# Optimization experiments

Hardware: AMD Instinct MI355X
Metric: run time of the kernel (lower is better)

## Reference

```python
import jax, jax.numpy as jnp
import numpy as np

N = 50000      # nodes
E = 1600000    # edges (avg degree 32)
D = 64         # d_node
DE = 32        # d_edge
H = 4          # heads
L = 3          # layers


def _ln(x, g, b):
    mu = x.mean(-1, keepdims=True)
    var = ((x - mu) ** 2).mean(-1, keepdims=True)
    return (x - mu) / jnp.sqrt(var + 1e-5) * g + b


def setup_inputs() -> dict:
    key = jax.random.key(0)
    ks = jax.random.split(key, 16)
    s = 0.05
    return {
        "node_features": jax.random.normal(ks[0], (N, D), jnp.float32),
        "edge_features": jax.random.normal(ks[1], (E, DE), jnp.float32),
        "edge_index": jax.random.randint(ks[2], (2, E), 0, N),
        "Wq": jax.random.normal(ks[3], (L, D, D), jnp.float32) * s,
        "Wk": jax.random.normal(ks[4], (L, D, D), jnp.float32) * s,
        "Wv": jax.random.normal(ks[5], (L, D, D), jnp.float32) * s,
        "Wo": jax.random.normal(ks[6], (L, D, D), jnp.float32) * s,
        "We": jax.random.normal(ks[7], (L, DE, H), jnp.float32) * s,   # edge-conditioned score bias
        "Wem": jax.random.normal(ks[8], (L, 2 * D + DE, DE), jnp.float32) * s,
        "bem": jnp.zeros((L, DE), jnp.float32),
        "gn": jnp.ones((L, D), jnp.float32),
        "bn": jnp.zeros((L, D), jnp.float32),
        "ge": jnp.ones((L, DE), jnp.float32),
        "be": jnp.zeros((L, DE), jnp.float32),
    }


def _delta_forward(h, e, src, dst, Wq, Wk, Wv, Wo, We, Wem, bem, gn, bn, ge, be):
    n = h.shape[0]
    dh = D // H
    for i in range(L):
        # --- node attention over edges (sparse, per-dst segment softmax) ---
        q = (h @ Wq[i]).reshape(n, H, dh)
        k = (h @ Wk[i]).reshape(n, H, dh)
        v = (h @ Wv[i]).reshape(n, H, dh)
        scores = jnp.einsum('ehd,ehd->eh', q[dst], k[src]) / jnp.sqrt(jnp.float32(dh))
        scores = scores + e @ We[i]                         # edge-conditioned bias [E,H]
        m = jax.ops.segment_max(scores, dst, num_segments=n)
        p = jnp.exp(scores - m[dst])
        denom = jax.ops.segment_sum(p, dst, num_segments=n)
        alpha = p / (denom[dst] + 1e-9)                      # [E,H]
        msg = (alpha[:, :, None] * v[src]).reshape(-1, D)    # [E,D]
        agg = jax.ops.segment_sum(msg, dst, num_segments=n)  # [N,D]
        h = _ln(h + agg @ Wo[i], gn[i], bn[i])
        # --- edge update conditioned on endpoint nodes ---
        emsg = jax.nn.gelu(jnp.concatenate([h[src], h[dst], e], axis=-1) @ Wem[i] + bem[i])
        e = _ln(e + emsg, ge[i], be[i])
    return h


def reference(node_features, edge_features, edge_index, Wq, Wk, Wv, Wo, We, Wem, bem, gn, bn, ge, be):
    src = edge_index[0]
    dst = edge_index[1]
    return _delta_forward(node_features, edge_features, src, dst,
                          Wq, Wk, Wv, Wo, We, Wem, bem, gn, bn, ge, be)
```

## Files before the change

### kernel.cpp

```cpp
#include <hip/hip_runtime.h>
#include <hip/hip_bf16.h>
#include <math.h>

#define NN 50000
#define NE 1600000
#define D 64
#define DE 32
#define H 4
#define DH 16
#define L 3

typedef __attribute__((ext_vector_type(8))) short bf16x8;
typedef __attribute__((ext_vector_type(8))) short s16x8;
typedef __attribute__((ext_vector_type(4))) float f32x4;

__device__ __forceinline__ short f2b(float f) {
    __hip_bfloat16 h = __float2bfloat16(f);
    short s;
    __builtin_memcpy(&s, &h, 2);
    return s;
}
__device__ __forceinline__ float b2f(unsigned short u) {
    unsigned int x = ((unsigned int)u) << 16;
    float f; __builtin_memcpy(&f, &x, 4); return f;
}
__device__ __forceinline__ float b2f_lo(unsigned int p) {
    unsigned int x = p << 16;
    float f; __builtin_memcpy(&f, &x, 4); return f;
}
__device__ __forceinline__ float b2f_hi(unsigned int p) {
    unsigned int x = p & 0xffff0000u;
    float f; __builtin_memcpy(&f, &x, 4); return f;
}


__global__ void deg_kernel(const int* __restrict__ dst, int* __restrict__ cnt) {
    int e = blockIdx.x * 256 + threadIdx.x;
    if (e >= NE) return;
    atomicAdd(&cnt[dst[e]], 1);
}

__global__ void block_sum_kernel(const int* __restrict__ cnt, int* __restrict__ bsum) {
    int b = blockIdx.x, t = threadIdx.x;
    int base = b * 1024 + t * 4;
    int s = 0;
#pragma unroll
    for (int i = 0; i < 4; i++) { int idx = base + i; if (idx < NN) s += cnt[idx]; }
#pragma unroll
    for (int off = 32; off; off >>= 1) s += __shfl_down(s, off);
    __shared__ int wsum[4];
    if ((t & 63) == 0) wsum[t >> 6] = s;
    __syncthreads();
    if (t == 0) bsum[b] = wsum[0] + wsum[1] + wsum[2] + wsum[3];
}

__global__ void scan_bsum_kernel(int* __restrict__ bsum, int nb) {
    if (blockIdx.x == 0 && threadIdx.x == 0) {
        int run = 0;
        for (int i = 0; i < nb; i++) { int c = bsum[i]; bsum[i] = run; run += c; }
    }
}

__global__ void scan_block_kernel(const int* __restrict__ cnt, const int* __restrict__ bsum,
                                  int* __restrict__ offsets) {
    int b = blockIdx.x, t = threadIdx.x;
    int base = b * 1024 + t * 4;
    int v[4]; int s = 0;
#pragma unroll
    for (int i = 0; i < 4; i++) { int idx = base + i; v[i] = (idx < NN) ? cnt[idx] : 0; s += v[i]; }
    int lane = t & 63, w = t >> 6;
    int x = s;
#pragma unroll
    for (int off = 1; off < 64; off <<= 1) {
        int y = __shfl_up(x, off);
        if (lane >= off) x += y;
    }
    __shared__ int wsum[4];
    if (lane == 63) wsum[w] = x;
    __syncthreads();
    int woff = 0;
    for (int i = 0; i < w; i++) woff += wsum[i];
    int run = bsum[b] + woff + x - s;
#pragma unroll
    for (int i = 0; i < 4; i++) {
        int idx = base + i;
        if (idx < NN) offsets[idx] = run;
        run += v[i];
    }
}

__global__ void scatter_kernel(const int* __restrict__ src, const int* __restrict__ dst,
                               const int* __restrict__ offsets,
                               int* __restrict__ cursor,
                               int* __restrict__ sorted_eid,
                               int* __restrict__ sorted_src,
                               int* __restrict__ sorted_dst) {
    int e = blockIdx.x * 256 + threadIdx.x;
    if (e >= NE) return;
    int d0 = dst[e];
    int pos = atomicAdd(&cursor[d0], 1);
    int position = offsets[d0] + pos;
    sorted_eid[position] = e;
    sorted_src[position] = src[e];
    sorted_dst[position] = d0;
}

__global__ void eperm_kernel(const float* __restrict__ e32, const int* __restrict__ sorted_eid,
                             const float* __restrict__ We0,
                             unsigned short* __restrict__ eb_s,
                             float* __restrict__ ebias_s) {
    int t = blockIdx.x * 256 + threadIdx.x;
    if (t >= NE * 4) return;
    int p = t >> 2;
    int c = (t & 3) * 8;
    int eid = sorted_eid[p];
    const float* ep = e32 + (size_t)eid * DE + c;
    float4 x0 = *(const float4*)(ep);
    float4 x1 = *(const float4*)(ep + 4);
    float e8[8] = {x0.x, x0.y, x0.z, x0.w, x1.x, x1.y, x1.z, x1.w};
    s16x8 ob;
#pragma unroll
    for (int i = 0; i < 8; i++) ob[i] = f2b(e8[i]);
    *(s16x8*)(eb_s + (size_t)p * DE + c) = ob;
    float p0 = 0.f, p1 = 0.f, p2 = 0.f, p3 = 0.f;
#pragma unroll
    for (int i = 0; i < 8; i++) {
        float4 w = *(const float4*)(We0 + (c + i) * 4);
        p0 += e8[i] * w.x; p1 += e8[i] * w.y; p2 += e8[i] * w.z; p3 += e8[i] * w.w;
    }
#pragma unroll
    for (int off = 1; off < 4; off <<= 1) {
        p0 += __shfl_xor(p0, off, 4);
        p1 += __shfl_xor(p1, off, 4);
        p2 += __shfl_xor(p2, off, 4);
        p3 += __shfl_xor(p3, off, 4);
    }
    if ((t & 3) == 0) {
        float4 o; o.x = p0; o.y = p1; o.z = p2; o.w = p3;
        *(float4*)(ebias_s + (size_t)p * H) = o;
    }
}

__global__ void wconv_kernel(const float* __restrict__ Wem, unsigned short* __restrict__ Wt) {
    int t = blockIdx.x * 256 + threadIdx.x;
    if (t >= L * 32 * 160) return;
    int l = t / 5120;
    int r = t % 5120;
    int n = r / 160;
    int k = r % 160;
    Wt[t] = (unsigned short)f2b(Wem[l * 5120 + k * 32 + n]);
}

__global__ void hconv_kernel(const float* __restrict__ nf, float* __restrict__ h,
                             unsigned short* __restrict__ hb) {
    int t = blockIdx.x * 256 + threadIdx.x;
    if (t >= NN * D) return;
    float x = nf[t];
    h[t] = x;
    hb[t] = (unsigned short)f2b(x);
}


__global__ void qkv_kernel(const float* __restrict__ h,
                           const float* __restrict__ Wq,
                           const float* __restrict__ Wk,
                           const float* __restrict__ Wv,
                           float* __restrict__ q, unsigned int* __restrict__ kv) {
    __shared__ float sW[3 * 4096];
    __shared__ float sh[16][D];
    int col = threadIdx.x;
    int wv = threadIdx.y;
    int tid = wv * 64 + col;
    int base = blockIdx.x * 16;
    for (int i = tid; i < 4096; i += 256) {
        sW[i] = Wq[i]; sW[4096 + i] = Wk[i]; sW[8192 + i] = Wv[i];
    }
    for (int i = tid; i < 16 * D; i += 256) {
        int n = base + (i >> 6);
        sh[i >> 6][i & 63] = h[n * D + (i & 63)];
    }
    __syncthreads();
#pragma unroll
    for (int it = 0; it < 4; it++) {
        int ln = wv * 4 + it;
        int node = base + ln;
        float aq = 0.f, ak = 0.f, av = 0.f;
#pragma unroll
        for (int kk = 0; kk < D; kk++) {
            float hv = sh[ln][kk];
            aq += hv * sW[kk * D + col];
            ak += hv * sW[4096 + kk * D + col];
            av += hv * sW[8192 + kk * D + col];
        }
        q[node * D + col] = aq * 0.25f;
        unsigned int kb = (unsigned int)(unsigned short)f2b(ak);
        unsigned int vb = (unsigned int)(unsigned short)f2b(av);
        kv[node * D + col] = (vb << 16) | kb;
    }
}

__global__ void attn_kernel(const float* __restrict__ q, const unsigned int* __restrict__ kv,
                            const float* __restrict__ ebias_s,
                            const int* __restrict__ sorted_src,
                            const int* __restrict__ offsets,
                            float* __restrict__ agg) {
    int node = blockIdx.x * 4 + threadIdx.y;
    node = __builtin_amdgcn_readfirstlane(node);
    if (node >= NN) return;
    int lane = threadIdx.x;
    int hh = lane >> 4;
    float qv = q[node * D + lane];
    int beg = offsets[node];
    int end = (node == NN - 1) ? NE : offsets[node + 1];
    float mmax = -INFINITY, den = 0.f, acc = 0.f;
    int i = beg;
    for (; i + 8 <= end; i += 8) {
        int ss[8]; unsigned int kk8[8]; float bb8[8], dd[8];
#pragma unroll
        for (int u = 0; u < 8; u++) ss[u] = sorted_src[i + u];
#pragma unroll
        for (int u = 0; u < 8; u++) kk8[u] = kv[ss[u] * D + lane];
#pragma unroll
        for (int u = 0; u < 8; u++) bb8[u] = ebias_s[(i + u) * H + hh];
#pragma unroll
        for (int u = 0; u < 8; u++) dd[u] = qv * b2f_lo(kk8[u]);
#pragma unroll
        for (int off = 1; off < 16; off <<= 1) {
#pragma unroll
            for (int u = 0; u < 8; u++) dd[u] += __shfl_xor(dd[u], off, 16);
        }
        float nm = mmax;
#pragma unroll
        for (int u = 0; u < 8; u++) { dd[u] += bb8[u]; nm = fmaxf(nm, dd[u]); }
        float scale = __expf(mmax - nm);
        float ps = 0.f, av = 0.f;
#pragma unroll
        for (int u = 0; u < 8; u++) {
            float p = __expf(dd[u] - nm);
            ps += p;
            av += p * b2f_hi(kk8[u]);
        }
        den = den * scale + ps;
        acc = acc * scale + av;
        mmax = nm;
    }
    for (; i < end; i++) {
        int s = sorted_src[i];
        unsigned int kvv = kv[s * D + lane];
        float b = ebias_s[i * H + hh];
        float dot = qv * b2f_lo(kvv);
#pragma unroll
        for (int off = 1; off < 16; off <<= 1) dot += __shfl_xor(dot, off, 16);
        float score = dot + b;
        float nm = fmaxf(mmax, score);
        float scale = __expf(mmax - nm);
        float p = __expf(score - nm);
        den = den * scale + p;
        acc = acc * scale + p * b2f_hi(kvv);
        mmax = nm;
    }
    agg[node * D + lane] = acc / (den + 1e-9f);
}

__global__ void node_update_kernel(float* __restrict__ h, const float* __restrict__ agg,
                                   const float* __restrict__ Wo,
                                   const float* __restrict__ gn,
                                   const float* __restrict__ bn,
                                   unsigned short* __restrict__ hb) {
    __shared__ float sWo[4096];
    __shared__ float sagg[16][D];
    int col = threadIdx.x, wv = threadIdx.y;
    int tid = wv * 64 + col;
    int base = blockIdx.x * 16;
    for (int i = tid; i < 4096; i += 256) sWo[i] = Wo[i];
    for (int i = tid; i < 16 * D; i += 256) {
        int n = base + (i >> 6);
        sagg[i >> 6][i & 63] = agg[n * D + (i & 63)];
    }
    __syncthreads();
    float gcol = gn[col], bcol = bn[col];
#pragma unroll
    for (int it = 0; it < 4; it++) {
        int ln = wv * 4 + it;
        int node = base + ln;
        float acc = 0.f;
#pragma unroll
        for (int kk = 0; kk < D; kk++) acc += sagg[ln][kk] * sWo[kk * D + col];
        float x = h[node * D + col] + acc;
        float sum = x, sq = x * x;
#pragma unroll
        for (int off = 32; off; off >>= 1) {
            sum += __shfl_xor(sum, off);
            sq += __shfl_xor(sq, off);
        }
        float mu = sum * (1.f / 64.f);
        float var = sq * (1.f / 64.f) - mu * mu;
        float out = (x - mu) * rsqrtf(var + 1e-5f) * gcol + bcol;
        h[node * D + col] = out;
        hb[node * D + col] = (unsigned short)f2b(out);
    }
}

__global__ void edge_update_mfma_kernel(const unsigned short* __restrict__ hb,
                                        unsigned short* __restrict__ eb_s,
                                        const int* __restrict__ sorted_src,
                                        const int* __restrict__ sorted_dst,
                                        const unsigned short* __restrict__ Wt,
                                        const float* __restrict__ bem,
                                        const float* __restrict__ ge,
                                        const float* __restrict__ be,
                                        const float* __restrict__ We_next,
                                        float* __restrict__ ebias_s,
                                        int do_bias, int do_estore) {
    int wave = threadIdx.x >> 6;
    int lane = threadIdx.x & 63;
    int we = blockIdx.x * 64 + wave * 16;
    int m = lane & 15;
    int quad = lane >> 4;
    int p_m = we + m;
    int s_idx = sorted_src[p_m], d_idx = sorted_dst[p_m];

    const unsigned short* as = hb + (size_t)s_idx * D + quad * 8;
    const unsigned short* ad = hb + (size_t)d_idx * D + quad * 8;
    const unsigned short* w0 = Wt + m * 160 + quad * 8;

    f32x4 c0 = {0.f, 0.f, 0.f, 0.f};
    f32x4 c1 = {0.f, 0.f, 0.f, 0.f};

#pragma unroll
    for (int ks = 0; ks < 4; ks++) {
        const unsigned short* ap = (ks < 2) ? as : ad;
        bf16x8 a = *(const bf16x8*)(ap + (ks & 1) * 32);
        bf16x8 b0 = *(const bf16x8*)(w0 + ks * 32);
        bf16x8 b1 = *(const bf16x8*)(w0 + ks * 32 + 16 * 160);
        c0 = __builtin_amdgcn_mfma_f32_16x16x32_bf16(a, b0, c0, 0, 0, 0);
        c1 = __builtin_amdgcn_mfma_f32_16x16x32_bf16(a, b1, c1, 0, 0, 0);
    }
    {
        bf16x8 a = *(const bf16x8*)(eb_s + (size_t)p_m * DE + quad * 8);
        bf16x8 b0 = *(const bf16x8*)(w0 + 4 * 32);
        bf16x8 b1 = *(const bf16x8*)(w0 + 4 * 32 + 16 * 160);
        c0 = __builtin_amdgcn_mfma_f32_16x16x32_bf16(a, b0, c0, 0, 0, 0);
        c1 = __builtin_amdgcn_mfma_f32_16x16x32_bf16(a, b1, c1, 0, 0, 0);
    }

    float bm0 = bem[m], bm1 = bem[m + 16];
    float g0 = ge[m], g1 = ge[m + 16];
    float bb0 = be[m], bb1 = be[m + 16];
    float4 wn0 = {0, 0, 0, 0}, wn1 = {0, 0, 0, 0};
    if (do_bias) {
        wn0 = *(const float4*)(We_next + m * 4);
        wn1 = *(const float4*)(We_next + (m + 16) * 4);
    }
#pragma unroll
    for (int reg = 0; reg < 4; reg++) {
        int er = we + quad * 4 + reg;
        float y0 = c0[reg] + bm0;
        float y1 = c1[reg] + bm1;
        float u0 = 1.5957691216057308f * (y0 + 0.044715f * y0 * y0 * y0);
        float u1 = 1.5957691216057308f * (y1 + 0.044715f * y1 * y1 * y1);
        float t0 = 1.f - 2.f / (1.f + __expf(u0));
        float t1 = 1.f - 2.f / (1.f + __expf(u1));
        y0 = 0.5f * y0 * (1.f + t0);
        y1 = 0.5f * y1 * (1.f + t1);
        float eo0 = b2f(eb_s[(size_t)er * DE + m]);
        float eo1 = b2f(eb_s[(size_t)er * DE + m + 16]);
        y0 += eo0;
        y1 += eo1;
        float s = y0 + y1, sq = y0 * y0 + y1 * y1;
#pragma unroll
        for (int off = 1; off < 16; off <<= 1) {
            s += __shfl_xor(s, off, 16);
            sq += __shfl_xor(sq, off, 16);
        }
        float mu = s * (1.f / 32.f);
        float var = sq * (1.f / 32.f) - mu * mu;
        float inv = rsqrtf(var + 1e-5f);
        float z0 = (y0 - mu) * inv * g0 + bb0;
        float z1 = (y1 - mu) * inv * g1 + bb1;
        if (do_estore) {
            eb_s[(size_t)er * DE + m] = (unsigned short)f2b(z0);
            eb_s[(size_t)er * DE + m + 16] = (unsigned short)f2b(z1);
        }
        if (do_bias) {
            float p0 = z0 * wn0.x + z1 * wn1.x;
            float p1 = z0 * wn0.y + z1 * wn1.y;
            float p2 = z0 * wn0.z + z1 * wn1.z;
            float p3 = z0 * wn0.w + z1 * wn1.w;
#pragma unroll
            for (int off = 1; off < 16; off <<= 1) {
                p0 += __shfl_xor(p0, off, 16);
                p1 += __shfl_xor(p1, off, 16);
                p2 += __shfl_xor(p2, off, 16);
                p3 += __shfl_xor(p3, off, 16);
            }
            if (m < 4) {
                float bsel = (m == 0) ? p0 : (m == 1) ? p1 : (m == 2) ? p2 : p3;
                ebias_s[er * H + m] = bsel;
            }
        }
    }
}

extern "C" void kernel_launch(void* const* d_in, const int* in_sizes, int n_in,
                              void* d_out, int out_size, void* d_ws, size_t ws_size,
                              hipStream_t stream) {
    const float* node_features = (const float*)d_in[0];
    const float* e = (const float*)d_in[1];
    const int* edge_index = (const int*)d_in[2];
    const int* src = edge_index;
    const int* dst = edge_index + NE;
    const float* Wq = (const float*)d_in[3];
    const float* Wk = (const float*)d_in[4];
    const float* Wv = (const float*)d_in[5];
    const float* Wo = (const float*)d_in[6];
    const float* We = (const float*)d_in[7];
    const float* Wem = (const float*)d_in[8];
    const float* bem = (const float*)d_in[9];
    const float* gn = (const float*)d_in[10];
    const float* bn = (const float*)d_in[11];
    const float* ge = (const float*)d_in[12];
    const float* be = (const float*)d_in[13];

    float* h = (float*)d_out;

    float* ws = (float*)d_ws;
    float* q = ws;
    unsigned int* kv = (unsigned int*)(q + NN * D);
    float* agg = (float*)(kv + NN * D);
    float* ebias_s = agg + NN * D;
    int* offsets = (int*)(ebias_s + (size_t)NE * H);
    int* cursor = offsets + NN;
    int* bsum = cursor + NN;
    int* sorted_eid = bsum + 64;
    int* sorted_src = sorted_eid + NE;
    int* sorted_dst = sorted_src + NE;
    unsigned short* Wt = (unsigned short*)(sorted_dst + NE);
    unsigned short* hb = Wt + L * 32 * 160;
    unsigned short* eb_s = hb + NN * D;

    const int NB = (NN + 1023) / 1024;

    hipMemsetAsync(cursor, 0, NN * sizeof(int), stream);
    deg_kernel<<<(NE + 255) / 256, 256, 0, stream>>>(dst, cursor);
    block_sum_kernel<<<NB, 256, 0, stream>>>(cursor, bsum);
    scan_bsum_kernel<<<1, 64, 0, stream>>>(bsum, NB);
    scan_block_kernel<<<NB, 256, 0, stream>>>(cursor, bsum, offsets);
    hipMemsetAsync(cursor, 0, NN * sizeof(int), stream);
    scatter_kernel<<<(NE + 255) / 256, 256, 0, stream>>>(src, dst, offsets, cursor,
                                                         sorted_eid, sorted_src, sorted_dst);
    eperm_kernel<<<(NE * 4 + 255) / 256, 256, 0, stream>>>(e, sorted_eid, We, eb_s, ebias_s);
    wconv_kernel<<<(L * 32 * 160 + 255) / 256, 256, 0, stream>>>(Wem, Wt);
    hconv_kernel<<<(NN * D + 255) / 256, 256, 0, stream>>>(node_features, h, hb);

    for (int layer = 0; layer < L; layer++) {
        const float* Wq_l = Wq + layer * D * D;
        const float* Wk_l = Wk + layer * D * D;
        const float* Wv_l = Wv + layer * D * D;
        const float* Wo_l = Wo + layer * D * D;
        const unsigned short* Wt_l = Wt + layer * 32 * 160;
        const float* bem_l = bem + layer * DE;
        const float* gn_l = gn + layer * D;
        const float* bn_l = bn + layer * D;
        const float* ge_l = ge + layer * DE;
        const float* be_l = be + layer * DE;

        qkv_kernel<<<NN / 16, dim3(64, 4), 0, stream>>>(h, Wq_l, Wk_l, Wv_l, q, kv);
        attn_kernel<<<NN / 4, dim3(64, 4), 0, stream>>>(q, kv, ebias_s, sorted_src,
                                                        offsets, agg);
        node_update_kernel<<<NN / 16, dim3(64, 4), 0, stream>>>(h, agg, Wo_l,
                                                                gn_l, bn_l, hb);
        if (layer < L - 1) {
            const float* We_next = We + (layer + 1) * DE * H;
            edge_update_mfma_kernel<<<NE / 64, 256, 0, stream>>>(hb, eb_s, sorted_src,
                                                                 sorted_dst, Wt_l,
                                                                 bem_l, ge_l, be_l,
                                                                 We_next, ebias_s,
                                                                 1, layer == 0 ? 1 : 0);
        }
    }
}
```

Measured before the change: 1.276 ms.

## Transpose edge-update output via LDS, vectorize LayerNorm and compute bias with MFMA

The GELU output is staged through shared memory and transposed so each lane holds 8 contiguous features of one edge. This lets the residual reuse the already-loaded edge vector, the LayerNorm reduction drop to two cross-lane shuffles, and the store become one 16-byte write per lane instead of scattered 2-byte writes. The next-layer score bias is now computed with a single bf16 MFMA against a zero-padded weight fragment, replacing the 16-lane shuffle reductions. The cost is an LDS round trip plus a block-wide barrier, and the bias is now computed from bf16-rounded values.

```diff
diff --git a/kernel.cpp b/kernel.cpp
--- a/kernel.cpp
+++ b/kernel.cpp
@@ -312,6 +312,7 @@
                                         const float* __restrict__ We_next,
                                         float* __restrict__ ebias_s,
                                         int do_bias, int do_estore) {
+    __shared__ __align__(16) float ytr[4][16][36];
     int wave = threadIdx.x >> 6;
     int lane = threadIdx.x & 63;
     int we = blockIdx.x * 64 + wave * 16;
@@ -324,6 +325,13 @@
     const unsigned short* ad = hb + (size_t)d_idx * D + quad * 8;
     const unsigned short* w0 = Wt + m * 160 + quad * 8;
 
+    bf16x8 wb;
+#pragma unroll
+    for (int j = 0; j < 8; j++) {
+        float w = (do_bias && m < 4) ? We_next[(quad * 8 + j) * 4 + m] : 0.f;
+        wb[j] = f2b(w);
+    }
+
     f32x4 c0 = {0.f, 0.f, 0.f, 0.f};
     f32x4 c1 = {0.f, 0.f, 0.f, 0.f};
 
@@ -336,67 +344,67 @@
         c0 = __builtin_amdgcn_mfma_f32_16x16x32_bf16(a, b0, c0, 0, 0, 0);
         c1 = __builtin_amdgcn_mfma_f32_16x16x32_bf16(a, b1, c1, 0, 0, 0);
     }
+    bf16x8 ea = *(const bf16x8*)(eb_s + (size_t)p_m * DE + quad * 8);
     {
-        bf16x8 a = *(const bf16x8*)(eb_s + (size_t)p_m * DE + quad * 8);
         bf16x8 b0 = *(const bf16x8*)(w0 + 4 * 32);
         bf16x8 b1 = *(const bf16x8*)(w0 + 4 * 32 + 16 * 160);
-        c0 = __builtin_amdgcn_mfma_f32_16x16x32_bf16(a, b0, c0, 0, 0, 0);
-        c1 = __builtin_amdgcn_mfma_f32_16x16x32_bf16(a, b1, c1, 0, 0, 0);
+        c0 = __builtin_amdgcn_mfma_f32_16x16x32_bf16(ea, b0, c0, 0, 0, 0);
+        c1 = __builtin_amdgcn_mfma_f32_16x16x32_bf16(ea, b1, c1, 0, 0, 0);
     }
 
     float bm0 = bem[m], bm1 = bem[m + 16];
-    float g0 = ge[m], g1 = ge[m + 16];
-    float bb0 = be[m], bb1 = be[m + 16];
-    float4 wn0 = {0, 0, 0, 0}, wn1 = {0, 0, 0, 0};
-    if (do_bias) {
-        wn0 = *(const float4*)(We_next + m * 4);
-        wn1 = *(const float4*)(We_next + (m + 16) * 4);
-    }
 #pragma unroll
     for (int reg = 0; reg < 4; reg++) {
-        int er = we + quad * 4 + reg;
+        int row = quad * 4 + reg;
         float y0 = c0[reg] + bm0;
         float y1 = c1[reg] + bm1;
         float u0 = 1.5957691216057308f * (y0 + 0.044715f * y0 * y0 * y0);
         float u1 = 1.5957691216057308f * (y1 + 0.044715f * y1 * y1 * y1);
         float t0 = 1.f - 2.f / (1.f + __expf(u0));
         float t1 = 1.f - 2.f / (1.f + __expf(u1));
-        y0 = 0.5f * y0 * (1.f + t0);
-        y1 = 0.5f * y1 * (1.f + t1);
-        float eo0 = b2f(eb_s[(size_t)er * DE + m]);
-        float eo1 = b2f(eb_s[(size_t)er * DE + m + 16]);
-        y0 += eo0;
-        y1 += eo1;
-        float s = y0 + y1, sq = y0 * y0 + y1 * y1;
-#pragma unroll
-        for (int off = 1; off < 16; off <<= 1) {
-            s += __shfl_xor(s, off, 16);
-            sq += __shfl_xor(sq, off, 16);
-        }
-        float mu = s * (1.f / 32.f);
-        float var = sq * (1.f / 32.f) - mu * mu;
-        float inv = rsqrtf(var + 1e-5f);
-        float z0 = (y0 - mu) * inv * g0 + bb0;
-        float z1 = (y1 - mu) * inv * g1 + bb1;
-        if (do_estore) {
-            eb_s[(size_t)er * DE + m] = (unsigned short)f2b(z0);
-            eb_s[(size_t)er * DE + m + 16] = (unsigned short)f2b(z1);
-        }
-        if (do_bias) {
-            float p0 = z0 * wn0.x + z1 * wn1.x;
-            float p1 = z0 * wn0.y + z1 * wn1.y;
-            float p2 = z0 * wn0.z + z1 * wn1.z;
-            float p3 = z0 * wn0.w + z1 * wn1.w;
-#pragma unroll
-            for (int off = 1; off < 16; off <<= 1) {
-                p0 += __shfl_xor(p0, off, 16);
-                p1 += __shfl_xor(p1, off, 16);
-                p2 += __shfl_xor(p2, off, 16);
-                p3 += __shfl_xor(p3, off, 16);
-            }
-            if (m < 4) {
-                float bsel = (m == 0) ? p0 : (m == 1) ? p1 : (m == 2) ? p2 : p3;
-                ebias_s[er * H + m] = bsel;
+        ytr[wave][row][m] = 0.5f * y0 * (1.f + t0);
+        ytr[wave][row][m + 16] = 0.5f * y1 * (1.f + t1);
+    }
+    __syncthreads();
+
+    float y[8];
+    *(f32x4*)&y[0] = *(const f32x4*)&ytr[wave][m][quad * 8];
+    *(f32x4*)&y[4] = *(const f32x4*)&ytr[wave][m][quad * 8 + 4];
+    float s = 0.f, sq = 0.f;
+#pragma unroll
+    for (int j = 0; j < 8; j++) {
+        y[j] += b2f((unsigned short)ea[j]);
+        s += y[j];
+        sq += y[j] * y[j];
+    }
+    s += __shfl_xor(s, 16); s += __shfl_xor(s, 32);
+    sq += __shfl_xor(sq, 16); sq += __shfl_xor(sq, 32);
+    float mu = s * (1.f / 32.f);
+    float var = sq * (1.f / 32.f) - mu * mu;
+    float inv = rsqrtf(var + 1e-5f);
+
+    float4 g0 = *(const float4*)(ge + quad * 8);
+    float4 g1 = *(const float4*)(ge + quad * 8 + 4);
+    float4 b0 = *(const float4*)(be + quad * 8);
+    float4 b1 = *(const float4*)(be + quad * 8 + 4);
+    float gg[8] = {g0.x, g0.y, g0.z, g0.w, g1.x, g1.y, g1.z, g1.w};
+    float bbv[8] = {b0.x, b0.y, b0.z, b0.w, b1.x, b1.y, b1.z, b1.w};
+    bf16x8 zb;
+#pragma unroll
+    for (int j = 0; j < 8; j++) {
+        float z = (y[j] - mu) * inv * gg[j] + bbv[j];
+        zb[j] = f2b(z);
+    }
+    if (do_estore) {
+        *(s16x8*)(eb_s + (size_t)p_m * DE + quad * 8) = zb;
+    }
+    if (do_bias) {
+        f32x4 db = {0.f, 0.f, 0.f, 0.f};
+        db = __builtin_amdgcn_mfma_f32_16x16x32_bf16(zb, wb, db, 0, 0, 0);
+        if (m < 4) {
+#pragma unroll
+            for (int reg = 0; reg < 4; reg++) {
+                ebias_s[(we + quad * 4 + reg) * H + m] = db[reg];
             }
         }
     }
```

After: 1.276 ms. Within noise of the previous version (-0.0%).
